# Kernel optimization log

Hardware: AMD Instinct MI355X
Metric: run time of the kernel (lower is better)

## Reference

```python
import jax, jax.numpy as jnp
import numpy as np

D_MODEL = 1024
HEADS = 16
D_K = D_MODEL // HEADS
D_FF = 4096
EPS = 1e-6


def setup_inputs() -> dict:
    key = jax.random.key(0)
    ks = jax.random.split(key, 16)
    s = 1.0 / np.sqrt(D_MODEL)
    inp = {
        'x': jax.random.normal(ks[0], (4, 2048, D_MODEL), dtype=jnp.float32),
        'Wq': jax.random.normal(ks[1], (D_MODEL, D_MODEL), dtype=jnp.float32) * s,
        'bq': jnp.zeros((D_MODEL,), jnp.float32),
        'Wk': jax.random.normal(ks[2], (D_MODEL, D_MODEL), dtype=jnp.float32) * s,
        'bk': jnp.zeros((D_MODEL,), jnp.float32),
        'Wv': jax.random.normal(ks[3], (D_MODEL, D_MODEL), dtype=jnp.float32) * s,
        'bv': jnp.zeros((D_MODEL,), jnp.float32),
        'Wo': jax.random.normal(ks[4], (D_MODEL, D_MODEL), dtype=jnp.float32) * s,
        'bo': jnp.zeros((D_MODEL,), jnp.float32),
        'alpha1': jnp.ones((D_MODEL,), jnp.float32),
        'bias1': jnp.zeros((D_MODEL,), jnp.float32),
        'alpha2': jnp.ones((D_MODEL,), jnp.float32),
        'bias2': jnp.zeros((D_MODEL,), jnp.float32),
        'W1': jax.random.normal(ks[5], (D_MODEL, D_FF), dtype=jnp.float32) * s,
        'b1': jnp.zeros((D_FF,), jnp.float32),
        'W2': jax.random.normal(ks[6], (D_FF, D_MODEL), dtype=jnp.float32) * (1.0 / np.sqrt(D_FF)),
        'b2': jnp.zeros((D_MODEL,), jnp.float32),
    }
    return inp


def _residual_norm(x, residual, alpha, bias):
    # x = x + residual; norm with mean and UNBIASED std (torch x.std default),
    # eps added to std (not variance), affine alpha/bias. Dropout = identity (eval).
    s = x + residual
    mean = jnp.mean(s, axis=-1, keepdims=True)
    std = jnp.std(s, axis=-1, keepdims=True, ddof=1)
    return alpha * (s - mean) / (std + EPS) + bias


def _forward(x, Wq, bq, Wk, bk, Wv, bv, Wo, bo, alpha1, bias1, alpha2, bias2, W1, b1, W2, b2):
    B, S, D = x.shape
    # QKV projections and head split: (B, H, S, d_k)
    def split_heads(t):
        return t.reshape(B, S, HEADS, D_K).transpose(0, 2, 1, 3)
    Q = split_heads(x @ Wq + bq)
    K = split_heads(x @ Wk + bk)
    V = split_heads(x @ Wv + bv)
    # scaled dot-product attention (no mask, no dropout in eval)
    scores = jnp.einsum('bhqd,bhkd->bhqk', Q, K) / np.sqrt(D_K)
    weights = jax.nn.softmax(scores, axis=-1)
    attn = jnp.einsum('bhqk,bhkd->bhqd', weights, V)
    concat = attn.transpose(0, 2, 1, 3).reshape(B, S, D)
    attn_out = concat @ Wo + bo
    # post-norm residual 1
    norm1 = _residual_norm(attn_out, x, alpha1, bias1)
    # FFN (dropout = identity in eval)
    ff = jax.nn.relu(norm1 @ W1 + b1) @ W2 + b2
    # post-norm residual 2
    return _residual_norm(ff, norm1, alpha2, bias2)


def reference(x, Wq, bq, Wk, bk, Wv, bv, Wo, bo, alpha1, bias1, alpha2, bias2, W1, b1, W2, b2):
    return _forward(x, Wq, bq, Wk, bk, Wv, bv, Wo, bo, alpha1, bias1, alpha2, bias2, W1, b1, W2, b2)
```

## Files before the change

kernel.cpp:

```cpp
#include <hip/hip_runtime.h>
#include <hip/hip_bf16.h>
#include <stdint.h>

typedef __attribute__((ext_vector_type(8))) short bv8;
typedef __attribute__((ext_vector_type(4))) short sv4;
typedef __attribute__((ext_vector_type(4))) float f4;
typedef __attribute__((ext_vector_type(4))) unsigned uv4;

#define LDS_AS __attribute__((address_space(3)))
#define GLB_AS __attribute__((address_space(1)))

#if __has_builtin(__builtin_amdgcn_exp2f)
#define EXP2F(x) __builtin_amdgcn_exp2f(x)
#else
#define EXP2F(x) exp2f(x)
#endif

#define GBAR __builtin_amdgcn_s_barrier()

__device__ __forceinline__ void gload16(const void* g, void* l) {
  __builtin_amdgcn_global_load_lds((GLB_AS void*)(g), (LDS_AS void*)(l), 16, 0, 0);
}

__device__ __forceinline__ short f2bs(float x) {
  return __builtin_bit_cast(short, __float2bfloat16(x));
}
__device__ __forceinline__ float bs2f(short s) {
  unsigned u = ((unsigned)(unsigned short)s) << 16;
  return __builtin_bit_cast(float, u);
}
__device__ __forceinline__ unsigned cvtpk(float lo, float hi) {
  unsigned r;
  asm("v_cvt_pk_bf16_f32 %0, %1, %2" : "=v"(r) : "v"(lo), "v"(hi));
  return r;
}

__global__ __launch_bounds__(256) void k_cvt(const float* __restrict__ in, short* __restrict__ out) {
  const int i = (blockIdx.x * 256 + threadIdx.x) * 4;
  const float4 v = *(const float4*)(in + i);
  sv4 o; o[0] = f2bs(v.x); o[1] = f2bs(v.y); o[2] = f2bs(v.z); o[3] = f2bs(v.w);
  *(sv4*)(out + i) = o;
}

__global__ __launch_bounds__(256) void k_transpose(const float* __restrict__ W, short* __restrict__ Wt,
                                                   int K, int N) {
  __shared__ float tile[32][33];
  const int tx = threadIdx.x & 31, ty = threadIdx.x >> 5;
  const int n0 = blockIdx.x * 32, k0 = blockIdx.y * 32;
#pragma unroll
  for (int i = 0; i < 32; i += 8)
    tile[ty + i][tx] = W[(size_t)(k0 + ty + i) * N + n0 + tx];
  __syncthreads();
#pragma unroll
  for (int i = 0; i < 32; i += 8)
    Wt[(size_t)(n0 + ty + i) * K + k0 + tx] = f2bs(tile[tx][ty + i]);
}

template<int EPI, int MIH>
__global__ __launch_bounds__(512) void k_gemm8p(
    const short* __restrict__ A, const short* __restrict__ Bt,
    const float* __restrict__ bias, const float* __restrict__ bias2, const float* __restrict__ bias3,
    short* __restrict__ C, short* __restrict__ D2, short* __restrict__ D3,
    int M, int N, int K, int nbx) {
  constexpr int BM = MIH * 64;
  constexpr int HOFF = (MIH == 4) ? 16384 : 4096;
  __shared__ __align__(16) short SA[2][BM * 64];
  __shared__ __align__(16) short SB[2][256 * 64];

  const int t = threadIdx.x;
  const int lane = t & 63, w = t >> 6;
  const int wr = w >> 2, wc = w & 3;
  const int lr = lane & 15, lg = lane >> 4;
  const int cpx = gridDim.x >> 3;
  const int bid = blockIdx.x;
  const int wid = (bid & 7) * cpx + (bid >> 3);
  const int by = wid / nbx, bx = wid % nbx;
  const int m0 = by * BM, n0 = bx * 256;
  const int nt = K >> 6;
  const int swz = ((t >> 3) & 7) << 4;
  const int rbyte0 = (lg * 16) ^ ((lr & 7) << 4);
  const int rbyte1 = (64 + lg * 16) ^ ((lr & 7) << 4);

  auto ST_A = [&](int k0, int half, int buf) {
#pragma unroll
    for (int i = 0; i < 2; ++i) {
      const int L = t * 16 + i * 8192;
      const int cbs = (L & 127) ^ swz;
      const int grow = (MIH == 4) ? (m0 + i * 128 + half * 64 + (t >> 3))
                                  : (m0 + i * 64 + (t >> 3));
      gload16(A + (size_t)grow * K + k0 + (cbs >> 1),
              (char*)SA[buf] + (MIH == 4 ? half * 16384 : 0) + L);
    }
  };
  auto ST_B = [&](int k0, int half, int buf) {
#pragma unroll
    for (int i = 0; i < 2; ++i) {
      const int L = t * 16 + i * 8192;
      const int rr = (t >> 3) + i * 64;
      const int cbs = (L & 127) ^ swz;
      const int grow = n0 + (rr >> 5) * 64 + half * 32 + (rr & 31);
      gload16(Bt + (size_t)grow * K + k0 + (cbs >> 1),
              (char*)SB[buf] + half * 16384 + L);
    }
  };

  f4 acc[2 * MIH][4] = {};
  bv8 af[MIH][2], bflo[2][2], bfhi[2][2];

  auto LDA = [&](int buf, int half) {
    const char* base = (const char*)SA[buf] + half * HOFF + wr * 8192;
#pragma unroll
    for (int m = 0; m < MIH; ++m) {
      af[m][0] = *(const bv8*)(base + (m * 16 + lr) * 128 + rbyte0);
      af[m][1] = *(const bv8*)(base + (m * 16 + lr) * 128 + rbyte1);
    }
  };
  auto LDB = [&](int buf, int half, bv8 (&bf)[2][2]) {
    const char* base = (const char*)SB[buf] + half * 16384 + wc * 4096;
#pragma unroll
    for (int n = 0; n < 2; ++n) {
      bf[n][0] = *(const bv8*)(base + (n * 16 + lr) * 128 + rbyte0);
      bf[n][1] = *(const bv8*)(base + (n * 16 + lr) * 128 + rbyte1);
    }
  };
  auto MM = [&](bv8 (&bf)[2][2], int mB, int nB) {
    __builtin_amdgcn_s_setprio(1);
#pragma unroll
    for (int kk = 0; kk < 2; ++kk)
#pragma unroll
      for (int m = 0; m < MIH; ++m)
#pragma unroll
        for (int n = 0; n < 2; ++n)
          acc[mB + m][nB + n] = __builtin_amdgcn_mfma_f32_16x16x32_bf16(
              af[m][kk], bf[n][kk], acc[mB + m][nB + n], 0, 0, 0);
    __builtin_amdgcn_s_setprio(0);
  };

  ST_A(0, 0, 0); if (MIH == 4) ST_A(0, 1, 0);
  ST_B(0, 0, 0); ST_B(0, 1, 0);
  ST_A(64, 0, 1);
  ST_B(64, 1, 1);
  if (MIH == 4) { ST_A(64, 1, 1); asm volatile("s_waitcnt vmcnt(6)" ::: "memory"); }
  else          { asm volatile("s_waitcnt vmcnt(4)" ::: "memory"); }
  GBAR;

  const int nIter = nt >> 1;
  for (int it = 0; it < nIter; ++it) {
    const int k1 = (2 * it + 1) << 6;
    const int k2 = (2 * it + 2) << 6, k3 = (2 * it + 3) << 6;
    const bool h2 = (2 * it + 2) < nt, h3 = (2 * it + 3) < nt;

    LDA(0, 0); LDB(0, 0, bflo);
    ST_B(k1, 0, 1);
    GBAR; MM(bflo, 0, 0); GBAR;
    LDB(0, 1, bfhi);
    if (h2 && MIH == 4) ST_A(k2, 0, 0);
    GBAR; MM(bfhi, 0, 2); GBAR;
    LDA(0, 1);
    if (h2) ST_B(k2, 1, 0);
    GBAR; MM(bfhi, MIH, 2); GBAR;
    if (h2) ST_A(k2, (MIH == 4) ? 1 : 0, 0);
    if (h2) {
      if (MIH == 4) asm volatile("s_waitcnt vmcnt(6)" ::: "memory");
      else          asm volatile("s_waitcnt vmcnt(4)" ::: "memory");
    } else {
      asm volatile("s_waitcnt vmcnt(0)" ::: "memory");
    }
    GBAR; MM(bflo, MIH, 0); GBAR;

    LDA(1, 0); LDB(1, 0, bflo);
    if (h2) ST_B(k2, 0, 0);
    GBAR; MM(bflo, 0, 0); GBAR;
    LDB(1, 1, bfhi);
    if (h3 && MIH == 4) ST_A(k3, 0, 1);
    GBAR; MM(bfhi, 0, 2); GBAR;
    LDA(1, 1);
    if (h3) ST_B(k3, 1, 1);
    GBAR; MM(bfhi, MIH, 2); GBAR;
    if (h3) ST_A(k3, (MIH == 4) ? 1 : 0, 1);
    if (h3) {
      if (MIH == 4) asm volatile("s_waitcnt vmcnt(6)" ::: "memory");
      else          asm volatile("s_waitcnt vmcnt(4)" ::: "memory");
    } else {
      asm volatile("s_waitcnt vmcnt(0)" ::: "memory");
    }
    GBAR; MM(bflo, MIH, 0); GBAR;
  }

#pragma unroll
  for (int ni = 0; ni < 4; ++ni) {
    const int c = n0 + wc * 64 + ni * 16 + lr;
    float bvs;
    int sel = 0, h = 0, d = 0;
    if (EPI == 2) {
      sel = c >> 10; const int cc = c & 1023;
      bvs = (sel == 0 ? bias : sel == 1 ? bias2 : bias3)[cc];
      h = cc >> 6; d = cc & 63;
    } else {
      bvs = bias[c];
    }
#pragma unroll
    for (int mi = 0; mi < 2 * MIH; ++mi) {
#pragma unroll
      for (int j = 0; j < 4; ++j) {
        const int r = m0 + wr * (MIH * 32) + mi * 16 + lg * 4 + j;
        float v = acc[mi][ni][j] + bvs;
        if (EPI == 1) v = fmaxf(v, 0.f);
        if (EPI == 2) {
          const int bb = r >> 11, s = r & 2047;
          if (sel == 0)      C [((size_t)(bb * 16 + h) * 2048 + s) * 64 + d] = f2bs(v);
          else if (sel == 1) D2[((size_t)(bb * 16 + h) * 2048 + s) * 64 + d] = f2bs(v);
          else               D3[((size_t)(bb * 16 + h) * 64 + d) * 2048 + s] = f2bs(v);
        } else {
          C[(size_t)r * N + c] = f2bs(v);
        }
      }
    }
  }
}

__global__ __launch_bounds__(256) void k_attn(const short* __restrict__ Qg, const short* __restrict__ Kg,
                                              const short* __restrict__ Vtg, short* __restrict__ Oc) {
  __shared__ __align__(16) short Ks[2][128 * 64];

  const int t = threadIdx.x, lane = t & 63, w = t >> 6;
  const int lr = lane & 15, lg = lane >> 4;
  const int bid = blockIdx.x;
  const int wid = (bid & 7) * 128 + (bid >> 3);
  const int q0 = (wid & 15) * 128;
  const int bh = wid >> 4;
  const int b = bh >> 4, h = bh & 15;
  const short* Qp = Qg + (size_t)bh * 2048 * 64;
  const short* Kp = Kg + (size_t)bh * 2048 * 64;
  const short* Vp = Vtg + (size_t)bh * 64 * 2048;

  bv8 qf[2][2];
#pragma unroll
  for (int mi = 0; mi < 2; ++mi)
#pragma unroll
    for (int kk = 0; kk < 2; ++kk)
      qf[mi][kk] = *(const bv8*)(Qp + (size_t)(q0 + w * 32 + mi * 16 + lr) * 64 + kk * 32 + lg * 8);

  f4 Oa[2][4] = {};
  float lsum[2] = {0.f, 0.f};
  const float SC = 0.125f * 1.44269504089f;
  const bool hi = lg >= 2;
  const bool xx = (lg == 1) || (lg == 2);

#pragma unroll
  for (int i = 0; i < 4; ++i) {
    const int L = t * 16 + i * 4096;
    const int row = L >> 7;
    const int cbs = (L & 127) ^ ((row & 7) << 4);
    gload16(Kp + (size_t)row * 64 + (cbs >> 1), (char*)Ks[0] + L);
  }
  __syncthreads();

  int cur = 0;
  for (int kt = 0; kt < 2048; kt += 128) {
    if (kt + 128 < 2048) {
#pragma unroll
      for (int i = 0; i < 4; ++i) {
        const int L = t * 16 + i * 4096;
        const int row = L >> 7;
        const int cbs = (L & 127) ^ ((row & 7) << 4);
        gload16(Kp + (size_t)(kt + 128 + row) * 64 + (cbs >> 1), (char*)Ks[cur ^ 1] + L);
      }
    }
    const char* Kb = (const char*)Ks[cur];

#pragma unroll
    for (int hf = 0; hf < 2; ++hf) {
      f4 Sa[2][4] = {};
#pragma unroll
      for (int kk = 0; kk < 2; ++kk) {
        bv8 kf[4];
#pragma unroll
        for (int nl = 0; nl < 4; ++nl) {
          const int row = (hf * 4 + nl) * 16 + lr;
          const int cb = kk * 64 + lg * 16;
          kf[nl] = *(const bv8*)(Kb + row * 128 + (cb ^ ((row & 7) << 4)));
        }
        __builtin_amdgcn_s_setprio(1);
#pragma unroll
        for (int mi = 0; mi < 2; ++mi)
#pragma unroll
          for (int nl = 0; nl < 4; ++nl)
            Sa[mi][nl] = __builtin_amdgcn_mfma_f32_16x16x32_bf16(kf[nl], qf[mi][kk], Sa[mi][nl], 0, 0, 0);
        __builtin_amdgcn_s_setprio(0);
      }

#pragma unroll
      for (int mi = 0; mi < 2; ++mi) {
        float rs = 0.f;
#pragma unroll
        for (int nl = 0; nl < 4; ++nl)
#pragma unroll
          for (int j = 0; j < 4; ++j) {
            const float p = EXP2F(Sa[mi][nl][j] * SC);
            Sa[mi][nl][j] = p;
            rs += p;
          }
        lsum[mi] += rs;
      }

#pragma unroll
      for (int k2 = 0; k2 < 2; ++k2) {
        bv8 vf[4], pf[2];
#pragma unroll
        for (int nO = 0; nO < 4; ++nO)
          vf[nO] = *(const bv8*)(Vp + (size_t)(nO * 16 + lr) * 2048 + kt + hf * 64 + k2 * 32 + lg * 8);
#pragma unroll
        for (int mi = 0; mi < 2; ++mi) {
          const unsigned W0 = cvtpk(Sa[mi][2 * k2][0], Sa[mi][2 * k2][1]);
          const unsigned W1 = cvtpk(Sa[mi][2 * k2][2], Sa[mi][2 * k2][3]);
          const unsigned W2 = cvtpk(Sa[mi][2 * k2 + 1][0], Sa[mi][2 * k2 + 1][1]);
          const unsigned W3 = cvtpk(Sa[mi][2 * k2 + 1][2], Sa[mi][2 * k2 + 1][3]);
          const unsigned w0 = hi ? W2 : W0, w1 = hi ? W3 : W1;
          const unsigned s0 = __shfl_xor(hi ? W0 : W2, 32);
          const unsigned s1 = __shfl_xor(hi ? W1 : W3, 32);
          const unsigned t0 = __shfl_xor(xx ? w0 : s0, 16);
          const unsigned t1 = __shfl_xor(xx ? w1 : s1, 16);
          uv4 u;
          u[0] = (lg == 0) ? w0 : (lg == 2) ? s0 : t0;
          u[1] = (lg == 0) ? w1 : (lg == 2) ? s1 : t1;
          u[2] = (lg == 3) ? w0 : (lg == 1) ? s0 : t0;
          u[3] = (lg == 3) ? w1 : (lg == 1) ? s1 : t1;
          pf[mi] = __builtin_bit_cast(bv8, u);
        }
        __builtin_amdgcn_s_setprio(1);
#pragma unroll
        for (int mi = 0; mi < 2; ++mi)
#pragma unroll
          for (int nO = 0; nO < 4; ++nO)
            Oa[mi][nO] = __builtin_amdgcn_mfma_f32_16x16x32_bf16(vf[nO], pf[mi], Oa[mi][nO], 0, 0, 0);
        __builtin_amdgcn_s_setprio(0);
      }
    }

    __syncthreads();
    cur ^= 1;
  }

#pragma unroll
  for (int mi = 0; mi < 2; ++mi) {
    lsum[mi] += __shfl_xor(lsum[mi], 16);
    lsum[mi] += __shfl_xor(lsum[mi], 32);
  }

#pragma unroll
  for (int mi = 0; mi < 2; ++mi) {
    const float inv = 1.f / lsum[mi];
    const int q = q0 + w * 32 + mi * 16 + lr;
#pragma unroll
    for (int nO = 0; nO < 4; ++nO) {
      sv4 o;
#pragma unroll
      for (int j = 0; j < 4; ++j) o[j] = f2bs(Oa[mi][nO][j] * inv);
      const int c = h * 64 + nO * 16 + lg * 4;
      *(sv4*)(Oc + ((size_t)b * 2048 + q) * 1024 + c) = o;
    }
  }
}

template<int MODE>
__global__ __launch_bounds__(256) void k_resnorm(const short* __restrict__ a, const void* __restrict__ res,
                                                 const float* __restrict__ alpha, const float* __restrict__ beta,
                                                 void* __restrict__ out) {
  const int row = blockIdx.x;
  const int t = threadIdx.x;
  const int lane = t & 63, w = t >> 6;
  const size_t base = (size_t)row * 1024;

  const sv4 av = *(const sv4*)(a + base + t * 4);
  float v[4];
  if (MODE == 0) {
    const float4 rv = *(const float4*)((const float*)res + base + t * 4);
    v[0] = bs2f(av[0]) + rv.x; v[1] = bs2f(av[1]) + rv.y;
    v[2] = bs2f(av[2]) + rv.z; v[3] = bs2f(av[3]) + rv.w;
  } else {
    const sv4 rv = *(const sv4*)((const short*)res + base + t * 4);
#pragma unroll
    for (int i = 0; i < 4; ++i) v[i] = bs2f(av[i]) + bs2f(rv[i]);
  }
  float s = v[0] + v[1] + v[2] + v[3];
  float sq = v[0] * v[0] + v[1] * v[1] + v[2] * v[2] + v[3] * v[3];
#pragma unroll
  for (int m = 1; m < 64; m <<= 1) { s += __shfl_xor(s, m); sq += __shfl_xor(sq, m); }
  __shared__ float red[8];
  if (lane == 0) { red[w] = s; red[w + 4] = sq; }
  __syncthreads();
  s = red[0] + red[1] + red[2] + red[3];
  sq = red[4] + red[5] + red[6] + red[7];
  const float mean = s * (1.f / 1024.f);
  const float var = (sq - 1024.f * mean * mean) * (1.f / 1023.f);
  const float inv = 1.f / (sqrtf(fmaxf(var, 0.f)) + 1e-6f);
  const float4 al = *(const float4*)(alpha + t * 4);
  const float4 be = *(const float4*)(beta + t * 4);
  float y[4];
  y[0] = al.x * (v[0] - mean) * inv + be.x;
  y[1] = al.y * (v[1] - mean) * inv + be.y;
  y[2] = al.z * (v[2] - mean) * inv + be.z;
  y[3] = al.w * (v[3] - mean) * inv + be.w;
  if (MODE == 0) {
    sv4 o; o[0] = f2bs(y[0]); o[1] = f2bs(y[1]); o[2] = f2bs(y[2]); o[3] = f2bs(y[3]);
    *(sv4*)((short*)out + base + t * 4) = o;
  } else {
    *(float4*)((float*)out + base + t * 4) = make_float4(y[0], y[1], y[2], y[3]);
  }
}

extern "C" void kernel_launch(void* const* d_in, const int* in_sizes, int n_in,
                              void* d_out, int out_size, void* d_ws, size_t ws_size,
                              hipStream_t stream) {
  const float* x   = (const float*)d_in[0];
  const float* Wq  = (const float*)d_in[1];
  const float* bq  = (const float*)d_in[2];
  const float* Wk  = (const float*)d_in[3];
  const float* bk  = (const float*)d_in[4];
  const float* Wv  = (const float*)d_in[5];
  const float* bv  = (const float*)d_in[6];
  const float* Wo  = (const float*)d_in[7];
  const float* bo  = (const float*)d_in[8];
  const float* al1 = (const float*)d_in[9];
  const float* bi1 = (const float*)d_in[10];
  const float* al2 = (const float*)d_in[11];
  const float* bi2 = (const float*)d_in[12];
  const float* W1  = (const float*)d_in[13];
  const float* b1  = (const float*)d_in[14];
  const float* W2  = (const float*)d_in[15];
  const float* b2  = (const float*)d_in[16];

  if (ws_size < (size_t)136 * 1024 * 1024) return;

  char* ws = (char*)d_ws;
  short* xb  = (short*)(ws);
  short* Qb  = (short*)(ws + (16ll << 20));
  short* Kb  = (short*)(ws + (32ll << 20));
  short* Vtb = (short*)(ws + (48ll << 20));
  short* Hb  = (short*)(ws);
  short* Wqt = (short*)(ws + (64ll << 20));
  short* Wkt = (short*)(ws + (66ll << 20));
  short* Wvt = (short*)(ws + (68ll << 20));
  short* Wot = (short*)(ws + (70ll << 20));
  short* W1t = (short*)(ws + (72ll << 20));
  short* W2t = (short*)(ws + (80ll << 20));
  short* Cc  = (short*)(ws + (88ll << 20));
  short* AOb = (short*)(ws + (104ll << 20));
  short* N1b = (short*)(ws + (120ll << 20));
  short* FFb = (short*)(ws + (104ll << 20));

  k_cvt<<<8192, 256, 0, stream>>>(x, xb);
  k_transpose<<<dim3(32, 32), 256, 0, stream>>>(Wq, Wqt, 1024, 1024);
  k_transpose<<<dim3(32, 32), 256, 0, stream>>>(Wk, Wkt, 1024, 1024);
  k_transpose<<<dim3(32, 32), 256, 0, stream>>>(Wv, Wvt, 1024, 1024);
  k_transpose<<<dim3(32, 32), 256, 0, stream>>>(Wo, Wot, 1024, 1024);
  k_transpose<<<dim3(128, 32), 256, 0, stream>>>(W1, W1t, 1024, 4096);
  k_transpose<<<dim3(32, 128), 256, 0, stream>>>(W2, W2t, 4096, 1024);

  k_gemm8p<2, 2><<<768, 512, 0, stream>>>(xb, Wqt, bq, bk, bv, Qb, Kb, Vtb, 8192, 3072, 1024, 12);

  k_attn<<<1024, 256, 0, stream>>>(Qb, Kb, Vtb, Cc);

  k_gemm8p<0, 2><<<256, 512, 0, stream>>>(Cc, Wot, bo, nullptr, nullptr, AOb, nullptr, nullptr,
                                          8192, 1024, 1024, 4);
  k_resnorm<0><<<8192, 256, 0, stream>>>(AOb, x, al1, bi1, N1b);

  k_gemm8p<1, 4><<<512, 512, 0, stream>>>(N1b, W1t, b1, nullptr, nullptr, Hb, nullptr, nullptr,
                                          8192, 4096, 1024, 16);
  k_gemm8p<0, 2><<<256, 512, 0, stream>>>(Hb, W2t, b2, nullptr, nullptr, FFb, nullptr, nullptr,
                                          8192, 1024, 4096, 4);
  k_resnorm<1><<<8192, 256, 0, stream>>>(FFb, N1b, al2, bi2, (float*)d_out);
}
```

Measured before the change: 473.9 us.

## Merge prep kernels into one launch and software-pipeline attention V loads with QK

Folds the input bf16 conversion and six weight-transpose launches into a single k_prep kernel that dispatches on block index, removing six kernel launches and their tail gaps. In the attention kernel, the inner loop is reordered so V fragments for both halves are issued early and the second half's QK^T/softmax overlaps the first half's PV MFMAs. This raises register pressure, since two sets of V and P fragments stay live, which may lower occupancy.

```diff
diff --git a/kernel.cpp b/kernel.cpp
--- a/kernel.cpp
+++ b/kernel.cpp
@@ -35,18 +35,36 @@
   return r;
 }
 
-__global__ __launch_bounds__(256) void k_cvt(const float* __restrict__ in, short* __restrict__ out) {
-  const int i = (blockIdx.x * 256 + threadIdx.x) * 4;
-  const float4 v = *(const float4*)(in + i);
-  sv4 o; o[0] = f2bs(v.x); o[1] = f2bs(v.y); o[2] = f2bs(v.z); o[3] = f2bs(v.w);
-  *(sv4*)(out + i) = o;
-}
-
-__global__ __launch_bounds__(256) void k_transpose(const float* __restrict__ W, short* __restrict__ Wt,
-                                                   int K, int N) {
+__global__ __launch_bounds__(256) void k_prep(const float* __restrict__ x, short* __restrict__ xb,
+                                              const float* __restrict__ Wq, short* __restrict__ Wqt,
+                                              const float* __restrict__ Wk, short* __restrict__ Wkt,
+                                              const float* __restrict__ Wv, short* __restrict__ Wvt,
+                                              const float* __restrict__ Wo, short* __restrict__ Wot,
+                                              const float* __restrict__ W1, short* __restrict__ W1t,
+                                              const float* __restrict__ W2, short* __restrict__ W2t) {
+  const int bid = blockIdx.x;
+  if (bid < 8192) {
+    const int i = (bid * 256 + threadIdx.x) * 4;
+    const float4 v = *(const float4*)(x + i);
+    sv4 o; o[0] = f2bs(v.x); o[1] = f2bs(v.y); o[2] = f2bs(v.z); o[3] = f2bs(v.w);
+    *(sv4*)(xb + i) = o;
+    return;
+  }
+  const float* W; short* Wt; int K, N, l;
+  if (bid < 12288) {
+    l = (bid - 8192) & 1023; K = 1024; N = 1024;
+    const int sel = (bid - 8192) >> 10;
+    W  = sel == 0 ? Wq  : sel == 1 ? Wk  : sel == 2 ? Wv  : Wo;
+    Wt = sel == 0 ? Wqt : sel == 1 ? Wkt : sel == 2 ? Wvt : Wot;
+  } else if (bid < 16384) {
+    l = bid - 12288; K = 1024; N = 4096; W = W1; Wt = W1t;
+  } else {
+    l = bid - 16384; K = 4096; N = 1024; W = W2; Wt = W2t;
+  }
+  const int nb = N >> 5;
+  const int n0 = (l % nb) * 32, k0 = (l / nb) * 32;
   __shared__ float tile[32][33];
   const int tx = threadIdx.x & 31, ty = threadIdx.x >> 5;
-  const int n0 = blockIdx.x * 32, k0 = blockIdx.y * 32;
 #pragma unroll
   for (int i = 0; i < 32; i += 8)
     tile[ty + i][tx] = W[(size_t)(k0 + ty + i) * N + n0 + tx];
@@ -247,6 +265,78 @@
   const bool hi = lg >= 2;
   const bool xx = (lg == 1) || (lg == 2);
 
+  auto QKSM = [&](const char* Kb, int hf, bv8 (&pf)[2][2]) {
+    f4 Sa[2][4] = {};
+#pragma unroll
+    for (int kk = 0; kk < 2; ++kk) {
+      bv8 kf[4];
+#pragma unroll
+      for (int nl = 0; nl < 4; ++nl) {
+        const int row = (hf * 4 + nl) * 16 + lr;
+        const int cb = kk * 64 + lg * 16;
+        kf[nl] = *(const bv8*)(Kb + row * 128 + (cb ^ ((row & 7) << 4)));
+      }
+      __builtin_amdgcn_s_setprio(1);
+#pragma unroll
+      for (int mi = 0; mi < 2; ++mi)
+#pragma unroll
+        for (int nl = 0; nl < 4; ++nl)
+          Sa[mi][nl] = __builtin_amdgcn_mfma_f32_16x16x32_bf16(kf[nl], qf[mi][kk], Sa[mi][nl], 0, 0, 0);
+      __builtin_amdgcn_s_setprio(0);
+    }
+#pragma unroll
+    for (int mi = 0; mi < 2; ++mi) {
+      float rs = 0.f;
+#pragma unroll
+      for (int nl = 0; nl < 4; ++nl)
+#pragma unroll
+        for (int j = 0; j < 4; ++j) {
+          const float p = EXP2F(Sa[mi][nl][j] * SC);
+          Sa[mi][nl][j] = p;
+          rs += p;
+        }
+      lsum[mi] += rs;
+    }
+#pragma unroll
+    for (int k2 = 0; k2 < 2; ++k2)
+#pragma unroll
+      for (int mi = 0; mi < 2; ++mi) {
+        const unsigned W0 = cvtpk(Sa[mi][2 * k2][0], Sa[mi][2 * k2][1]);
+        const unsigned W1 = cvtpk(Sa[mi][2 * k2][2], Sa[mi][2 * k2][3]);
+        const unsigned W2 = cvtpk(Sa[mi][2 * k2 + 1][0], Sa[mi][2 * k2 + 1][1]);
+        const unsigned W3 = cvtpk(Sa[mi][2 * k2 + 1][2], Sa[mi][2 * k2 + 1][3]);
+        const unsigned w0 = hi ? W2 : W0, w1 = hi ? W3 : W1;
+        const unsigned s0 = __shfl_xor(hi ? W0 : W2, 32);
+        const unsigned s1 = __shfl_xor(hi ? W1 : W3, 32);
+        const unsigned t0 = __shfl_xor(xx ? w0 : s0, 16);
+        const unsigned t1 = __shfl_xor(xx ? w1 : s1, 16);
+        uv4 u;
+        u[0] = (lg == 0) ? w0 : (lg == 2) ? s0 : t0;
+        u[1] = (lg == 0) ? w1 : (lg == 2) ? s1 : t1;
+        u[2] = (lg == 3) ? w0 : (lg == 1) ? s0 : t0;
+        u[3] = (lg == 3) ? w1 : (lg == 1) ? s1 : t1;
+        pf[k2][mi] = __builtin_bit_cast(bv8, u);
+      }
+  };
+  auto LOADV = [&](int kt, int hf, bv8 (&vf)[2][4]) {
+#pragma unroll
+    for (int k2 = 0; k2 < 2; ++k2)
+#pragma unroll
+      for (int nO = 0; nO < 4; ++nO)
+        vf[k2][nO] = *(const bv8*)(Vp + (size_t)(nO * 16 + lr) * 2048 + kt + hf * 64 + k2 * 32 + lg * 8);
+  };
+  auto PV = [&](bv8 (&vf)[2][4], bv8 (&pf)[2][2]) {
+    __builtin_amdgcn_s_setprio(1);
+#pragma unroll
+    for (int k2 = 0; k2 < 2; ++k2)
+#pragma unroll
+      for (int mi = 0; mi < 2; ++mi)
+#pragma unroll
+        for (int nO = 0; nO < 4; ++nO)
+          Oa[mi][nO] = __builtin_amdgcn_mfma_f32_16x16x32_bf16(vf[k2][nO], pf[k2][mi], Oa[mi][nO], 0, 0, 0);
+    __builtin_amdgcn_s_setprio(0);
+  };
+
 #pragma unroll
   for (int i = 0; i < 4; ++i) {
     const int L = t * 16 + i * 4096;
@@ -269,74 +359,13 @@
     }
     const char* Kb = (const char*)Ks[cur];
 
-#pragma unroll
-    for (int hf = 0; hf < 2; ++hf) {
-      f4 Sa[2][4] = {};
-#pragma unroll
-      for (int kk = 0; kk < 2; ++kk) {
-        bv8 kf[4];
-#pragma unroll
-        for (int nl = 0; nl < 4; ++nl) {
-          const int row = (hf * 4 + nl) * 16 + lr;
-          const int cb = kk * 64 + lg * 16;
-          kf[nl] = *(const bv8*)(Kb + row * 128 + (cb ^ ((row & 7) << 4)));
-        }
-        __builtin_amdgcn_s_setprio(1);
-#pragma unroll
-        for (int mi = 0; mi < 2; ++mi)
-#pragma unroll
-          for (int nl = 0; nl < 4; ++nl)
-            Sa[mi][nl] = __builtin_amdgcn_mfma_f32_16x16x32_bf16(kf[nl], qf[mi][kk], Sa[mi][nl], 0, 0, 0);
-        __builtin_amdgcn_s_setprio(0);
-      }
-
-#pragma unroll
-      for (int mi = 0; mi < 2; ++mi) {
-        float rs = 0.f;
-#pragma unroll
-        for (int nl = 0; nl < 4; ++nl)
-#pragma unroll
-          for (int j = 0; j < 4; ++j) {
-            const float p = EXP2F(Sa[mi][nl][j] * SC);
-            Sa[mi][nl][j] = p;
-            rs += p;
-          }
-        lsum[mi] += rs;
-      }
-
-#pragma unroll
-      for (int k2 = 0; k2 < 2; ++k2) {
-        bv8 vf[4], pf[2];
-#pragma unroll
-        for (int nO = 0; nO < 4; ++nO)
-          vf[nO] = *(const bv8*)(Vp + (size_t)(nO * 16 + lr) * 2048 + kt + hf * 64 + k2 * 32 + lg * 8);
-#pragma unroll
-        for (int mi = 0; mi < 2; ++mi) {
-          const unsigned W0 = cvtpk(Sa[mi][2 * k2][0], Sa[mi][2 * k2][1]);
-          const unsigned W1 = cvtpk(Sa[mi][2 * k2][2], Sa[mi][2 * k2][3]);
-          const unsigned W2 = cvtpk(Sa[mi][2 * k2 + 1][0], Sa[mi][2 * k2 + 1][1]);
-          const unsigned W3 = cvtpk(Sa[mi][2 * k2 + 1][2], Sa[mi][2 * k2 + 1][3]);
-          const unsigned w0 = hi ? W2 : W0, w1 = hi ? W3 : W1;
-          const unsigned s0 = __shfl_xor(hi ? W0 : W2, 32);
-          const unsigned s1 = __shfl_xor(hi ? W1 : W3, 32);
-          const unsigned t0 = __shfl_xor(xx ? w0 : s0, 16);
-          const unsigned t1 = __shfl_xor(xx ? w1 : s1, 16);
-          uv4 u;
-          u[0] = (lg == 0) ? w0 : (lg == 2) ? s0 : t0;
-          u[1] = (lg == 0) ? w1 : (lg == 2) ? s1 : t1;
-          u[2] = (lg == 3) ? w0 : (lg == 1) ? s0 : t0;
-          u[3] = (lg == 3) ? w1 : (lg == 1) ? s1 : t1;
-          pf[mi] = __builtin_bit_cast(bv8, u);
-        }
-        __builtin_amdgcn_s_setprio(1);
-#pragma unroll
-        for (int mi = 0; mi < 2; ++mi)
-#pragma unroll
-          for (int nO = 0; nO < 4; ++nO)
-            Oa[mi][nO] = __builtin_amdgcn_mfma_f32_16x16x32_bf16(vf[nO], pf[mi], Oa[mi][nO], 0, 0, 0);
-        __builtin_amdgcn_s_setprio(0);
-      }
-    }
+    bv8 vfA[2][4], vfB[2][4], pfA[2][2], pfB[2][2];
+    LOADV(kt, 0, vfA);
+    QKSM(Kb, 0, pfA);
+    LOADV(kt, 1, vfB);
+    PV(vfA, pfA);
+    QKSM(Kb, 1, pfB);
+    PV(vfB, pfB);
 
     __syncthreads();
     cur ^= 1;
@@ -450,13 +479,7 @@
   short* N1b = (short*)(ws + (120ll << 20));
   short* FFb = (short*)(ws + (104ll << 20));
 
-  k_cvt<<<8192, 256, 0, stream>>>(x, xb);
-  k_transpose<<<dim3(32, 32), 256, 0, stream>>>(Wq, Wqt, 1024, 1024);
-  k_transpose<<<dim3(32, 32), 256, 0, stream>>>(Wk, Wkt, 1024, 1024);
-  k_transpose<<<dim3(32, 32), 256, 0, stream>>>(Wv, Wvt, 1024, 1024);
-  k_transpose<<<dim3(32, 32), 256, 0, stream>>>(Wo, Wot, 1024, 1024);
-  k_transpose<<<dim3(128, 32), 256, 0, stream>>>(W1, W1t, 1024, 4096);
-  k_transpose<<<dim3(32, 128), 256, 0, stream>>>(W2, W2t, 4096, 1024);
+  k_prep<<<20480, 256, 0, stream>>>(x, xb, Wq, Wqt, Wk, Wkt, Wv, Wvt, Wo, Wot, W1, W1t, W2, W2t);
 
   k_gemm8p<2, 2><<<768, 512, 0, stream>>>(xb, Wqt, bq, bk, bv, Qb, Kb, Vtb, 8192, 3072, 1024, 12);
 
```

After: 449.7 us. 5.1% less time.
